# Kernel tuning notes

Measured on AMD Instinct MI355X. Metric: run time of the kernel, lower is better.

Reference implementation:

```python
import jax, jax.numpy as jnp
import numpy as np

SIX = 6

def _make_table():
    # p_q_2_lut_table: [2*SIX, 2**SIX] binary selection matrix.
    # Flattened p_q order: indices 0..5 are (1-x)_j, indices 6..11 are x_j.
    t = np.zeros((2 * SIX, 2 ** SIX), dtype=np.float32)
    for i in range(2 ** SIX):
        bins = format(i, '06b')
        for j in range(SIX):
            if bins[j] == '0':
                t[j + SIX, i] = 1.0
            else:
                t[j, i] = 1.0
    return t

_P_Q_2_LUT_TABLE = jnp.asarray(_make_table())  # [12, 64]


def setup_inputs() -> dict:
    key = jax.random.key(0)
    k1, k2 = jax.random.split(key)
    B, N = 1024, 2048
    inputs = jax.random.uniform(k1, (B, N, SIX), dtype=jnp.float32)  # probabilities
    lut = jax.random.normal(k2, (N, 2 ** SIX), dtype=jnp.float32)
    return {"inputs": inputs, "lut": lut}


def reference(inputs, lut):
    eps = 1e-07
    # p_q: [B, N, 12] = concat(1 - x, x) along last axis (matches [2,6] flatten)
    p_q = jnp.concatenate([1.0 - inputs, inputs], axis=-1)
    p_q = jax.nn.relu(p_q) + eps
    p_q_log = jnp.log(p_q)
    # log-matmul-exp against binary selection table -> per-entry LUT probabilities
    lut_p = jnp.exp(jnp.einsum('bnk,kt->bnt', p_q_log, _P_Q_2_LUT_TABLE))  # [B,N,64]
    # weight by sigmoid(lut) [N,64] broadcast over batch, reduce over table axis
    output = jnp.sum(lut_p * jax.nn.sigmoid(lut)[None, :, :], axis=-1)  # [B,N]
    return output
```

## Files before the change

kernel.cpp:

```cpp
#include <hip/hip_runtime.h>

typedef float v2f __attribute__((ext_vector_type(2)));

__global__ __launch_bounds__(256, 4) void lut_kernel(const float* __restrict__ in,
                                                     const float* __restrict__ lut,
                                                     float* __restrict__ out,
                                                     int N) {
    __shared__ __align__(16) float wsm[64][68];

    const int t  = threadIdx.x;
    const int nl = t & 63;
    const int wv = t >> 6;
    const int n0 = blockIdx.x * 64;
    const int n  = n0 + nl;
    const int b0 = blockIdx.y * 32 + wv;

    {
        const float4* lp = reinterpret_cast<const float4*>(lut + (size_t)n0 * 64);
        const int rr = t >> 2, c4 = t & 3;
        #pragma unroll
        for (int p = 0; p < 4; ++p) {
            const int sidx = c4 + p * 4;
            float4 v = lp[rr * 16 + sidx];
            wsm[rr][sidx * 4 + 0] = 1.0f / (1.0f + __expf(-v.x));
            wsm[rr][sidx * 4 + 1] = 1.0f / (1.0f + __expf(-v.y));
            wsm[rr][sidx * 4 + 2] = 1.0f / (1.0f + __expf(-v.z));
            wsm[rr][sidx * 4 + 3] = 1.0f / (1.0f + __expf(-v.w));
        }
    }
    __syncthreads();

    v2f w2[32];
    #pragma unroll
    for (int k = 0; k < 16; ++k) {
        float4 v = *reinterpret_cast<const float4*>(&wsm[nl][k * 4]);
        w2[2 * k]     = (v2f){v.x, v.y};
        w2[2 * k + 1] = (v2f){v.z, v.w};
    }

    const float2* ip = reinterpret_cast<const float2*>(in) + ((size_t)b0 * N + n) * 3;
    const size_t st  = (size_t)N * 12;
    float* op = out + (size_t)b0 * N + n;

    float2 pf[2][3];
    pf[0][0] = ip[0];      pf[0][1] = ip[1];      pf[0][2] = ip[2];
    pf[1][0] = ip[st + 0]; pf[1][1] = ip[st + 1]; pf[1][2] = ip[st + 2];

    #pragma unroll
    for (int it = 0; it < 8; ++it) {
        const float2 va = pf[it & 1][0], vb = pf[it & 1][1], vc = pf[it & 1][2];
        if (it < 6) {
            const float2* np = ip + (size_t)(it + 2) * st;
            pf[it & 1][0] = np[0]; pf[it & 1][1] = np[1]; pf[it & 1][2] = np[2];
        }
        const float x0 = va.x, x1 = va.y, x2 = vb.x,
                    x3 = vb.y, x4 = vc.x, x5 = vc.y;
        const float B0 = 1.0f - x0, B1 = 1.0f - x1, B2 = 1.0f - x2,
                    B3 = 1.0f - x3, B4 = 1.0f - x4, B5 = 1.0f - x5;

        const float t01[4] = {x0 * x1, x0 * B1, B0 * x1, B0 * B1};
        const float t34[4] = {x3 * x4, x3 * B4, B3 * x4, B3 * B4};

        v2f tlo2[4];
        #pragma unroll
        for (int m = 0; m < 4; ++m)
            tlo2[m] = (v2f){t34[m] * x5, t34[m] * B5};

        v2f acc2 = (v2f){0.0f, 0.0f};
        #pragma unroll
        for (int h = 0; h < 8; ++h) {
            v2f s2 = tlo2[0] * w2[h * 4 + 0];
            s2 += tlo2[1] * w2[h * 4 + 1];
            s2 += tlo2[2] * w2[h * 4 + 2];
            s2 += tlo2[3] * w2[h * 4 + 3];
            const float th = t01[h >> 1] * ((h & 1) ? B2 : x2);
            acc2 += (v2f){th, th} * s2;
        }
        op[(size_t)it * 4 * N] = acc2.x + acc2.y;
    }
}

extern "C" void kernel_launch(void* const* d_in, const int* in_sizes, int n_in,
                              void* d_out, int out_size, void* d_ws, size_t ws_size,
                              hipStream_t stream) {
    const float* inputs = (const float*)d_in[0];
    const float* lut    = (const float*)d_in[1];
    float* out = (float*)d_out;

    const int lut_sz = in_sizes[1];
    const int N = lut_sz / 64;
    const int B = in_sizes[0] / (6 * N);

    dim3 grid(N / 64, B / 32);
    lut_kernel<<<grid, 256, 0, stream>>>(inputs, lut, out, N);
}
```

Baseline: 15.78 us.

## Use fp16 packed dot products for LUT weights and halve batch per block

Stores the sigmoid weights as fp16 in shared memory and registers. The inner contraction now uses v_dot2 fp16 instructions on packed pairs of the x4/x5 products, with fp32 accumulation over the outer factors. Each block now covers 16 batch rows instead of 32, so the grid doubles, and the launch bounds ask for 8 blocks per SM for more occupancy. The input prefetch moves ahead of the sigmoid staging to overlap global loads. Weights and partial products lose precision by rounding to fp16 with round-toward-zero, and each block repeats the sigmoid setup work twice as often.

```diff
diff --git a/kernel.cpp b/kernel.cpp
--- a/kernel.cpp
+++ b/kernel.cpp
@@ -1,55 +1,60 @@
 #include <hip/hip_runtime.h>
 
-typedef float v2f __attribute__((ext_vector_type(2)));
+typedef __fp16 h2 __attribute__((ext_vector_type(2)));
 
-__global__ __launch_bounds__(256, 4) void lut_kernel(const float* __restrict__ in,
+__global__ __launch_bounds__(256, 8) void lut_kernel(const float* __restrict__ in,
                                                      const float* __restrict__ lut,
                                                      float* __restrict__ out,
                                                      int N) {
-    __shared__ __align__(16) float wsm[64][68];
+    __shared__ __align__(16) __fp16 wsm[64][72];
 
     const int t  = threadIdx.x;
     const int nl = t & 63;
     const int wv = t >> 6;
     const int n0 = blockIdx.x * 64;
     const int n  = n0 + nl;
-    const int b0 = blockIdx.y * 32 + wv;
+    const int b0 = blockIdx.y * 16 + wv;
+
+    const float2* ip = reinterpret_cast<const float2*>(in) + ((size_t)b0 * N + n) * 3;
+    const size_t st  = (size_t)N * 12;
+    float2 pf[2][3];
+    pf[0][0] = ip[0];      pf[0][1] = ip[1];      pf[0][2] = ip[2];
+    pf[1][0] = ip[st + 0]; pf[1][1] = ip[st + 1]; pf[1][2] = ip[st + 2];
 
     {
         const float4* lp = reinterpret_cast<const float4*>(lut + (size_t)n0 * 64);
         const int rr = t >> 2, c4 = t & 3;
         #pragma unroll
         for (int p = 0; p < 4; ++p) {
-            const int sidx = c4 + p * 4;
-            float4 v = lp[rr * 16 + sidx];
-            wsm[rr][sidx * 4 + 0] = 1.0f / (1.0f + __expf(-v.x));
-            wsm[rr][sidx * 4 + 1] = 1.0f / (1.0f + __expf(-v.y));
-            wsm[rr][sidx * 4 + 2] = 1.0f / (1.0f + __expf(-v.z));
-            wsm[rr][sidx * 4 + 3] = 1.0f / (1.0f + __expf(-v.w));
+            const int s = c4 + p * 4;
+            float4 v = lp[rr * 16 + s];
+            h2 a = __builtin_amdgcn_cvt_pkrtz(1.0f / (1.0f + __expf(-v.x)),
+                                              1.0f / (1.0f + __expf(-v.y)));
+            h2 b = __builtin_amdgcn_cvt_pkrtz(1.0f / (1.0f + __expf(-v.z)),
+                                              1.0f / (1.0f + __expf(-v.w)));
+            *reinterpret_cast<h2*>(&wsm[rr][s * 4 + 0]) = a;
+            *reinterpret_cast<h2*>(&wsm[rr][s * 4 + 2]) = b;
         }
     }
     __syncthreads();
 
-    v2f w2[32];
+    h2 w2[32];
     #pragma unroll
-    for (int k = 0; k < 16; ++k) {
-        float4 v = *reinterpret_cast<const float4*>(&wsm[nl][k * 4]);
-        w2[2 * k]     = (v2f){v.x, v.y};
-        w2[2 * k + 1] = (v2f){v.z, v.w};
+    for (int k = 0; k < 8; ++k) {
+        h2 r0 = *reinterpret_cast<const h2*>(&wsm[nl][k * 8 + 0]);
+        h2 r1 = *reinterpret_cast<const h2*>(&wsm[nl][k * 8 + 2]);
+        h2 r2 = *reinterpret_cast<const h2*>(&wsm[nl][k * 8 + 4]);
+        h2 r3 = *reinterpret_cast<const h2*>(&wsm[nl][k * 8 + 6]);
+        w2[k * 4 + 0] = r0; w2[k * 4 + 1] = r1;
+        w2[k * 4 + 2] = r2; w2[k * 4 + 3] = r3;
     }
 
-    const float2* ip = reinterpret_cast<const float2*>(in) + ((size_t)b0 * N + n) * 3;
-    const size_t st  = (size_t)N * 12;
     float* op = out + (size_t)b0 * N + n;
 
-    float2 pf[2][3];
-    pf[0][0] = ip[0];      pf[0][1] = ip[1];      pf[0][2] = ip[2];
-    pf[1][0] = ip[st + 0]; pf[1][1] = ip[st + 1]; pf[1][2] = ip[st + 2];
-
     #pragma unroll
-    for (int it = 0; it < 8; ++it) {
+    for (int it = 0; it < 4; ++it) {
         const float2 va = pf[it & 1][0], vb = pf[it & 1][1], vc = pf[it & 1][2];
-        if (it < 6) {
+        if (it < 2) {
             const float2* np = ip + (size_t)(it + 2) * st;
             pf[it & 1][0] = np[0]; pf[it & 1][1] = np[1]; pf[it & 1][2] = np[2];
         }
@@ -58,25 +63,30 @@
         const float B0 = 1.0f - x0, B1 = 1.0f - x1, B2 = 1.0f - x2,
                     B3 = 1.0f - x3, B4 = 1.0f - x4, B5 = 1.0f - x5;
 
-        const float t01[4] = {x0 * x1, x0 * B1, B0 * x1, B0 * B1};
-        const float t34[4] = {x3 * x4, x3 * B4, B3 * x4, B3 * B4};
+        const float t01a[4] = {x0 * x1, x0 * B1, B0 * x1, B0 * B1};
+        const float t23a[4] = {x2 * x3, x2 * B3, B2 * x3, B2 * B3};
+        const h2 q0 = __builtin_amdgcn_cvt_pkrtz(x4 * x5, x4 * B5);
+        const h2 q1 = __builtin_amdgcn_cvt_pkrtz(B4 * x5, B4 * B5);
 
-        v2f tlo2[4];
+        float acc = 0.0f;
         #pragma unroll
-        for (int m = 0; m < 4; ++m)
-            tlo2[m] = (v2f){t34[m] * x5, t34[m] * B5};
-
-        v2f acc2 = (v2f){0.0f, 0.0f};
-        #pragma unroll
-        for (int h = 0; h < 8; ++h) {
-            v2f s2 = tlo2[0] * w2[h * 4 + 0];
-            s2 += tlo2[1] * w2[h * 4 + 1];
-            s2 += tlo2[2] * w2[h * 4 + 2];
-            s2 += tlo2[3] * w2[h * 4 + 3];
-            const float th = t01[h >> 1] * ((h & 1) ? B2 : x2);
-            acc2 += (v2f){th, th} * s2;
+        for (int g = 0; g < 4; ++g) {
+            float sg = 0.0f;
+            #pragma unroll
+            for (int j = 0; j < 4; ++j) {
+#if __has_builtin(__builtin_amdgcn_fdot2)
+                float d = __builtin_amdgcn_fdot2(q0, w2[g * 8 + j * 2 + 0], 0.0f, false);
+                d       = __builtin_amdgcn_fdot2(q1, w2[g * 8 + j * 2 + 1], d,    false);
+#else
+                const h2 wa = w2[g * 8 + j * 2 + 0], wb = w2[g * 8 + j * 2 + 1];
+                float d = (float)q0.x * (float)wa.x + (float)q0.y * (float)wa.y
+                        + (float)q1.x * (float)wb.x + (float)q1.y * (float)wb.y;
+#endif
+                sg = fmaf(t23a[j], d, sg);
+            }
+            acc = fmaf(t01a[g], sg, acc);
         }
-        op[(size_t)it * 4 * N] = acc2.x + acc2.y;
+        op[(size_t)it * 4 * N] = acc;
     }
 }
 
@@ -91,6 +101,6 @@
     const int N = lut_sz / 64;
     const int B = in_sizes[0] / (6 * N);
 
-    dim3 grid(N / 64, B / 32);
+    dim3 grid(N / 64, B / 16);
     lut_kernel<<<grid, 256, 0, stream>>>(inputs, lut, out, N);
 }
```

After: 16.18 us. +2.6%, slower.
